# Optimization experiments

Hardware: AMD Instinct MI355X
Metric: run time of the kernel (lower is better)

Reference implementation:

```python
import jax, jax.numpy as jnp
import numpy as np

B, S, HID = 1, 2048, 4096
NH, KVH, D = 32, 8, 128
MAXP = 2048
EPS = 1e-6


def _rope_tables(max_pos, dim, base=10000.0):
    inv_freq = 1.0 / (base ** (np.arange(0, dim, 2, dtype=np.float32) / dim))
    t = np.arange(max_pos, dtype=np.float32)
    freqs = np.outer(t, inv_freq)                      # [max_pos, dim/2]
    emb = np.concatenate([freqs, freqs], axis=-1)      # [max_pos, dim]
    return jnp.asarray(np.cos(emb)), jnp.asarray(np.sin(emb))


def setup_inputs() -> dict:
    key = jax.random.key(0)
    ks = jax.random.split(key, 6)
    x = jax.random.normal(ks[0], (B, S, HID), jnp.float32)
    scale = 0.02
    wq = jax.random.normal(ks[1], (NH * D, HID), jnp.float32) * scale
    wk = jax.random.normal(ks[2], (KVH * D, HID), jnp.float32) * scale
    wv = jax.random.normal(ks[3], (KVH * D, HID), jnp.float32) * scale
    wo = jax.random.normal(ks[4], (NH * D, HID), jnp.float32).T * scale  # stored as [HID, NH*D] -> transpose back
    wo = jnp.asarray(jax.random.normal(ks[4], (HID, NH * D), jnp.float32) * scale)
    cos_table, sin_table = _rope_tables(MAXP, D)
    return {
        "x": x, "wq": wq, "wk": wk, "wv": wv, "wo": wo,
        "q_norm_w": jnp.ones((D,), jnp.float32),
        "k_norm_w": jnp.ones((D,), jnp.float32),
        "cos_table": cos_table, "sin_table": sin_table,
        "k_cache": jnp.zeros((1, B, MAXP, KVH, D), jnp.float32),
        "v_cache": jnp.zeros((1, B, MAXP, KVH, D), jnp.float32),
        "positions": jnp.arange(S, dtype=jnp.int32),
        "layer_idx": 0,
    }


def _rmsnorm(x, w):
    return w * (x * jax.lax.rsqrt(jnp.mean(x * x, axis=-1, keepdims=True) + EPS))


def _rope(x, cos, sin):
    # x: [B, H, S, D]; cos/sin: [1, 1, S, D]
    half = x.shape[-1] // 2
    x1, x2 = x[..., :half], x[..., half:]
    rotated = jnp.concatenate([-x2, x1], axis=-1)
    return x * cos + rotated * sin


def reference(x, wq, wk, wv, wo, q_norm_w, k_norm_w, cos_table, sin_table,
              k_cache, v_cache, positions, layer_idx):
    bsz, seq_len, _ = x.shape
    d = q_norm_w.shape[0]
    nh = wq.shape[0] // d
    kvh = wk.shape[0] // d
    g = nh // kvh

    q = (x @ wq.T).reshape(bsz, seq_len, nh, d).transpose(0, 2, 1, 3)    # [B,NH,S,D]
    k = (x @ wk.T).reshape(bsz, seq_len, kvh, d).transpose(0, 2, 1, 3)   # [B,KVH,S,D]
    v = (x @ wv.T).reshape(bsz, seq_len, kvh, d).transpose(0, 2, 1, 3)

    q = _rmsnorm(q, q_norm_w)
    k = _rmsnorm(k, k_norm_w)

    cos = cos_table[positions][None, None]  # [1,1,S,D]
    sin = sin_table[positions][None, None]
    q = _rope(q, cos, sin)
    k = _rope(k, cos, sin)

    # KV-cache scatter at dynamic positions (prefill: positions = arange(S))
    kc = k_cache[layer_idx].at[:, positions].set(k.transpose(0, 2, 1, 3))
    vc = v_cache[layer_idx].at[:, positions].set(v.transpose(0, 2, 1, 3))
    # K = max(positions)+1 == seq_len in this (prefill) setup; static for jit
    K = seq_len
    k_all = kc[:, :K].transpose(0, 2, 1, 3)   # [B,KVH,K,D]
    v_all = vc[:, :K].transpose(0, 2, 1, 3)

    # GQA: group query heads instead of repeat_interleave on K/V (same math)
    qg = q.reshape(bsz, kvh, g, seq_len, d)
    scale = 1.0 / jnp.sqrt(jnp.asarray(d, q.dtype))
    scores = jnp.einsum('bkgqd,bkld->bkgql', qg, k_all) * scale
    causal = jnp.tril(jnp.ones((seq_len, K), dtype=bool))
    scores = jnp.where(causal, scores, jnp.finfo(scores.dtype).min)
    attn = jax.nn.softmax(scores, axis=-1)
    out = jnp.einsum('bkgql,bkld->bkgqd', attn, v_all)
    out = out.reshape(bsz, nh, seq_len, d).transpose(0, 2, 1, 3).reshape(bsz, seq_len, nh * d)
    return out @ wo.T
```

## Files before the change

### kernel.cpp

```cpp
#include <hip/hip_runtime.h>

typedef unsigned short u16;
typedef unsigned int u32;
typedef __attribute__((ext_vector_type(8))) short bf16x8;
typedef __attribute__((ext_vector_type(4))) float f32x4;
struct __align__(8) us4 { u16 x, y, z, w; };

#define S_LEN 2048
#define HID   4096
#define NH    32
#define KVH   8
#define HD    128
#define MFMA16 __builtin_amdgcn_mfma_f32_16x16x32_bf16

__device__ inline u16 f2bf(float f) {
  u32 u = __float_as_uint(f);
  u32 r = (u + 0x7fffu + ((u >> 16) & 1u)) >> 16;
  return (u16)r;
}
__device__ inline float bf2f(u16 h) { return __uint_as_float(((u32)h) << 16); }

__device__ inline void gld_lds16(const void* g, void* l) {
  __builtin_amdgcn_global_load_lds(
      (const __attribute__((address_space(1))) u32*)g,
      (__attribute__((address_space(3))) u32*)l, 16, 0, 0);
}

__global__ __launch_bounds__(256)
void cvt_all(const float* __restrict__ x, const float* __restrict__ wq,
             const float* __restrict__ wk, const float* __restrict__ wv,
             u16* __restrict__ xb, u16* __restrict__ wqb,
             u16* __restrict__ wkb, u16* __restrict__ wvb) {
  int b = blockIdx.x;
  const float* in; u16* out; int base;
  if (b < 8192)       { in = x;  out = xb;  base = b; }
  else if (b < 24576) { in = wq; out = wqb; base = b - 8192; }
  else if (b < 28672) { in = wk; out = wkb; base = b - 24576; }
  else                { in = wv; out = wvb; base = b - 28672; }
  size_t i = ((size_t)base * 256 + threadIdx.x) * 4;
  f32x4 v = *(const f32x4*)(in + i);
  us4 o;
  o.x = f2bf(v[0]); o.y = f2bf(v[1]); o.z = f2bf(v[2]); o.w = f2bf(v[3]);
  *(us4*)(out + i) = o;
}

__device__ __forceinline__ void stage_half(const u16* __restrict__ src, int ldk,
                                           int rowBase, int k0, char* lslot,
                                           int t) {
  int rl = t >> 3;
  int c8 = ((t & 7) ^ (rl & 7)) * 8;
  gld_lds16(src + (size_t)(rowBase + rl) * ldk + k0 + c8, lslot + t * 16);
  gld_lds16(src + (size_t)(rowBase + 64 + rl) * ldk + k0 + c8,
            lslot + 8192 + t * 16);
}

__device__ __forceinline__ void gemm256_core(
    const u16* __restrict__ A, const u16* __restrict__ W, int m0, int n0,
    int ldk, int kBeg, int kEnd, char* lds, f32x4 (&acc)[8][4]) {
  const int t = threadIdx.x;
  const int l = t & 63, w = t >> 6;
  const int l15 = l & 15, quad = l >> 4;
  const int wr = w >> 2, wcn = w & 3;
  const int nt = (kEnd - kBeg) >> 6;
  char* ldsA = lds;
  char* ldsB = lds + 65536;
  const int swz0 = ((0 + quad) ^ (l15 & 7)) * 16;
  const int swz1 = ((4 + quad) ^ (l15 & 7)) * 16;
  const int aB0 = wr * 16384 + l15 * 128;
  const int bB0 = wcn * 8192 + l15 * 128;

#pragma unroll
  for (int m = 0; m < 8; m++)
#pragma unroll
    for (int n = 0; n < 4; n++) acc[m][n] = (f32x4){0.f, 0.f, 0.f, 0.f};

  stage_half(W, ldk, n0,       kBeg, ldsB,         t);
  stage_half(W, ldk, n0 + 128, kBeg, ldsB + 16384, t);
  stage_half(A, ldk, m0,       kBeg, ldsA,         t);
  stage_half(A, ldk, m0 + 128, kBeg, ldsA + 16384, t);
  if (nt > 1) {
    stage_half(W, ldk, n0,       kBeg + 64, ldsB + 32768,         t);
    stage_half(W, ldk, n0 + 128, kBeg + 64, ldsB + 32768 + 16384, t);
    stage_half(A, ldk, m0,       kBeg + 64, ldsA + 32768,         t);
    stage_half(A, ldk, m0 + 128, kBeg + 64, ldsA + 32768 + 16384, t);
    asm volatile("s_waitcnt vmcnt(8)" ::: "memory");
  } else {
    asm volatile("s_waitcnt vmcnt(0)" ::: "memory");
  }
  __builtin_amdgcn_s_barrier();

  bf16x8 a[4][2], b[2][2], b2[2][2];
#pragma unroll 1
  for (int tt = 0; tt < nt; ++tt) {
    const int d = tt & 1;
    const int aO = d * 32768 + aB0;
    const int bO = d * 32768 + bB0;
    const int k2 = kBeg + (tt + 2) * 64;
    const bool pf = (tt + 2 < nt);

#pragma unroll
    for (int m = 0; m < 4; m++) {
      a[m][0] = *(const bf16x8*)(ldsA + aO + m * 2048 + swz0);
      a[m][1] = *(const bf16x8*)(ldsA + aO + m * 2048 + swz1);
    }
#pragma unroll
    for (int n = 0; n < 2; n++) {
      b[n][0] = *(const bf16x8*)(ldsB + bO + n * 2048 + swz0);
      b[n][1] = *(const bf16x8*)(ldsB + bO + n * 2048 + swz1);
    }
    __builtin_amdgcn_s_barrier();
    __builtin_amdgcn_s_setprio(1);
#pragma unroll
    for (int m = 0; m < 4; m++)
#pragma unroll
      for (int n = 0; n < 2; n++) {
        acc[m][n] = MFMA16(a[m][0], b[n][0], acc[m][n], 0, 0, 0);
        acc[m][n] = MFMA16(a[m][1], b[n][1], acc[m][n], 0, 0, 0);
      }
    __builtin_amdgcn_s_setprio(0);
    __builtin_amdgcn_s_barrier();

#pragma unroll
    for (int n = 0; n < 2; n++) {
      b2[n][0] = *(const bf16x8*)(ldsB + bO + (2 + n) * 2048 + swz0);
      b2[n][1] = *(const bf16x8*)(ldsB + bO + (2 + n) * 2048 + swz1);
    }
    __builtin_amdgcn_s_barrier();
    __builtin_amdgcn_s_setprio(1);
#pragma unroll
    for (int m = 0; m < 4; m++)
#pragma unroll
      for (int n = 0; n < 2; n++) {
        acc[m][2 + n] = MFMA16(a[m][0], b2[n][0], acc[m][2 + n], 0, 0, 0);
        acc[m][2 + n] = MFMA16(a[m][1], b2[n][1], acc[m][2 + n], 0, 0, 0);
      }
    __builtin_amdgcn_s_setprio(0);
    __builtin_amdgcn_s_barrier();

    if (pf) {
      stage_half(W, ldk, n0,       k2, ldsB + d * 32768,         t);
      stage_half(W, ldk, n0 + 128, k2, ldsB + d * 32768 + 16384, t);
    }
#pragma unroll
    for (int m = 0; m < 4; m++) {
      a[m][0] = *(const bf16x8*)(ldsA + aO + (4 + m) * 2048 + swz0);
      a[m][1] = *(const bf16x8*)(ldsA + aO + (4 + m) * 2048 + swz1);
    }
    __builtin_amdgcn_s_barrier();
    __builtin_amdgcn_s_setprio(1);
#pragma unroll
    for (int m = 0; m < 4; m++)
#pragma unroll
      for (int n = 0; n < 2; n++) {
        acc[4 + m][n] = MFMA16(a[m][0], b[n][0], acc[4 + m][n], 0, 0, 0);
        acc[4 + m][n] = MFMA16(a[m][1], b[n][1], acc[4 + m][n], 0, 0, 0);
      }
    __builtin_amdgcn_s_setprio(0);
    __builtin_amdgcn_s_barrier();

    if (pf) {
      stage_half(A, ldk, m0,       k2, ldsA + d * 32768,         t);
      stage_half(A, ldk, m0 + 128, k2, ldsA + d * 32768 + 16384, t);
    }
    __builtin_amdgcn_s_barrier();
    __builtin_amdgcn_s_setprio(1);
#pragma unroll
    for (int m = 0; m < 4; m++)
#pragma unroll
      for (int n = 0; n < 2; n++) {
        acc[4 + m][2 + n] = MFMA16(a[m][0], b2[n][0], acc[4 + m][2 + n], 0, 0, 0);
        acc[4 + m][2 + n] = MFMA16(a[m][1], b2[n][1], acc[4 + m][2 + n], 0, 0, 0);
      }
    __builtin_amdgcn_s_setprio(0);
    if (pf) asm volatile("s_waitcnt vmcnt(8)" ::: "memory");
    else    asm volatile("s_waitcnt vmcnt(0)" ::: "memory");
    __builtin_amdgcn_s_barrier();
  }
}

__global__ __launch_bounds__(512, 2)
void gemm_qkv8(const u16* __restrict__ xb, const u16* __restrict__ wqb,
               const u16* __restrict__ wkb, const u16* __restrict__ wvb,
               u16* __restrict__ Qp, u16* __restrict__ Kp, u16* __restrict__ vt,
               const float* __restrict__ wo, u16* __restrict__ wob) {
  extern __shared__ char lds[];
  const int id = blockIdx.x;
  if (id >= 192) {
    int cb = id - 192;
    size_t base = ((size_t)cb * 512 + threadIdx.x) * 4;
#pragma unroll 1
    for (int it = 0; it < 128; ++it) {
      size_t i = base + (size_t)it * 131072;
      f32x4 v = *(const f32x4*)(wo + i);
      us4 o;
      o.x = f2bf(v[0]); o.y = f2bf(v[1]); o.z = f2bf(v[2]); o.w = f2bf(v[3]);
      *(us4*)(wob + i) = o;
    }
    return;
  }
  const int sw = (id & 7) * 24 + (id >> 3);
  const int bx = sw % 24, by = sw / 24;
  const u16* W; u16* C; int n0, ldc, epi;
  if (bx < 16)      { W = wqb; C = Qp; n0 = bx * 256;        ldc = HID;  epi = 0; }
  else if (bx < 20) { W = wkb; C = Kp; n0 = (bx - 16) * 256; ldc = 1024; epi = 0; }
  else              { W = wvb; C = vt; n0 = (bx - 20) * 256; ldc = 0;    epi = 1; }
  const int m0 = by * 256;

  f32x4 acc[8][4];
  gemm256_core(xb, W, m0, n0, HID, 0, HID, lds, acc);

  const int t = threadIdx.x, l = t & 63, w = t >> 6;
  const int l15 = l & 15, quad = l >> 4;
  const int wr = w >> 2, wcn = w & 3;
  if (epi == 0) {
#pragma unroll
    for (int m = 0; m < 8; m++) {
      int row0 = m0 + wr * 128 + m * 16 + quad * 4;
#pragma unroll
      for (int n = 0; n < 4; n++) {
        int col = n0 + wcn * 64 + n * 16 + l15;
#pragma unroll
        for (int r = 0; r < 4; r++)
          C[(size_t)(row0 + r) * ldc + col] = f2bf(acc[m][n][r]);
      }
    }
  } else {
#pragma unroll
    for (int m = 0; m < 8; m++) {
      int row0 = m0 + wr * 128 + m * 16 + quad * 4;
#pragma unroll
      for (int n = 0; n < 4; n++) {
        int col = n0 + wcn * 64 + n * 16 + l15;
        us4 v;
        v.x = f2bf(acc[m][n][0]); v.y = f2bf(acc[m][n][1]);
        v.z = f2bf(acc[m][n][2]); v.w = f2bf(acc[m][n][3]);
        *(us4*)(vt + (size_t)col * S_LEN + row0) = v;
      }
    }
  }
}

__global__ __launch_bounds__(512, 2)
void gemm_out8(const u16* __restrict__ ab, const u16* __restrict__ wob,
               float* __restrict__ O0, float* __restrict__ O1) {
  extern __shared__ char lds[];
  const int id = blockIdx.x;
  const int sw = (id & 7) * 32 + (id >> 3);
  const int z = sw >> 7, rem = sw & 127;
  const int by = rem >> 4, bx = rem & 15;
  float* Op = z ? O1 : O0;

  f32x4 acc[8][4];
  gemm256_core(ab, wob, by * 256, bx * 256, HID, z * 2048, z * 2048 + 2048, lds, acc);

  const int t = threadIdx.x, l = t & 63, w = t >> 6;
  const int l15 = l & 15, quad = l >> 4;
  const int wr = w >> 2, wcn = w & 3;
#pragma unroll
  for (int m = 0; m < 8; m++) {
    int row0 = by * 256 + wr * 128 + m * 16 + quad * 4;
#pragma unroll
    for (int n = 0; n < 4; n++) {
      int col = bx * 256 + wcn * 64 + n * 16 + l15;
#pragma unroll
      for (int r = 0; r < 4; r++)
        Op[(size_t)(row0 + r) * HID + col] = acc[m][n][r];
    }
  }
}

__global__ __launch_bounds__(256)
void reduce_out(const float* __restrict__ O0, const float* __restrict__ O1,
                float* __restrict__ outp) {
  size_t i = ((size_t)blockIdx.x * 256 + threadIdx.x) * 4;
  f32x4 a = *(const f32x4*)(O0 + i);
  f32x4 b = *(const f32x4*)(O1 + i);
  a[0] += b[0]; a[1] += b[1]; a[2] += b[2]; a[3] += b[3];
  *(f32x4*)(outp + i) = a;
}

__global__ __launch_bounds__(256)
void rope_all(const u16* __restrict__ Qp, const u16* __restrict__ Kp,
              const float* __restrict__ qnw, const float* __restrict__ knw,
              const float* __restrict__ cosT, const float* __restrict__ sinT,
              const int* __restrict__ pos, u16* __restrict__ qbh,
              u16* __restrict__ kbh) {
  const int b = blockIdx.x;
  const int t = threadIdx.x, w = t >> 6, l = t & 63;
  const u16* xr; const float* nw; u16* orow; int s;
  if (b < 16384) {
    int p = b * 4 + w;
    s = p >> 5; int h = p & 31;
    xr = Qp + (size_t)s * HID + h * HD;
    nw = qnw;
    orow = qbh + ((size_t)h * S_LEN + s) * HD;
  } else {
    int p = (b - 16384) * 4 + w;
    s = p >> 3; int h = p & 7;
    xr = Kp + (size_t)s * 1024 + h * HD;
    nw = knw;
    orow = kbh + ((size_t)h * S_LEN + s) * HD;
  }
  float x1 = bf2f(xr[l]);
  float x2 = bf2f(xr[l + 64]);
  float ss = x1 * x1 + x2 * x2;
#pragma unroll
  for (int m = 1; m < 64; m <<= 1) ss += __shfl_xor(ss, m);
  float rinv = rsqrtf(ss * (1.0f / 128.0f) + 1e-6f);
  float n1 = x1 * rinv * nw[l];
  float n2 = x2 * rinv * nw[l + 64];
  int ps = pos[s];
  float c1 = cosT[ps * HD + l], s1 = sinT[ps * HD + l];
  float c2 = cosT[ps * HD + l + 64], s2 = sinT[ps * HD + l + 64];
  float y1 = n1 * c1 - n2 * s1;
  float y2 = n2 * c2 + n1 * s2;
  orow[l] = f2bf(y1);
  orow[l + 64] = f2bf(y2);
}

__global__ __launch_bounds__(256)
void attn_fwd(const u16* __restrict__ qh, const u16* __restrict__ kbh,
              const u16* __restrict__ vth, u16* __restrict__ ab) {
  __shared__ __align__(16) u16 lK[64 * 128];
  __shared__ __align__(16) u16 lV[128 * 64];
  __shared__ __align__(16) u16 lP[4][16 * 72];
  const int t = threadIdx.x, w = t >> 6, l = t & 63;
  const int quad = l >> 4, l15 = l & 15;
  const int h = blockIdx.x;
  const int qt = 31 - blockIdx.y;
  const int kvh = h >> 2;
  const int q0 = qt * 64;
  const int qrow = q0 + w * 16 + l15;

  bf16x8 qf[4];
#pragma unroll
  for (int ks = 0; ks < 4; ks++)
    qf[ks] = *(const bf16x8*)(qh + ((size_t)h * S_LEN + qrow) * HD + ks * 32 + quad * 8);

  f32x4 accO[8];
#pragma unroll
  for (int j = 0; j < 8; j++) accO[j] = (f32x4){0.f, 0.f, 0.f, 0.f};
  float m_cur = -3.0e38f, l_sum = 0.f;
  const float scale = 0.08838834764831845f;

  const int ntiles = qt + 1;
  for (int tt = 0; tt < ntiles; tt++) {
    const int c0 = tt * 64;
#pragma unroll
    for (int i = 0; i < 4; i++) {
      int Cc = i * 256 + t;
      int r = Cc >> 4, ch = Cc & 15;
      int gch = ch ^ (r & 15);
      gld_lds16(kbh + ((size_t)kvh * S_LEN + c0 + r) * HD + gch * 8, lK + Cc * 8);
    }
#pragma unroll
    for (int i = 0; i < 4; i++) {
      int Cc = i * 256 + t;
      int d = Cc >> 3, ch = Cc & 7;
      int gch = ch ^ (d & 7);
      gld_lds16(vth + ((size_t)kvh * HD + d) * S_LEN + c0 + gch * 8, lV + Cc * 8);
    }
    __syncthreads();

    f32x4 st[4];
#pragma unroll
    for (int i = 0; i < 4; i++) {
      f32x4 sa = (f32x4){0.f, 0.f, 0.f, 0.f};
      int r = i * 16 + l15;
#pragma unroll
      for (int ks = 0; ks < 4; ks++) {
        int lc = ks * 4 + quad;
        bf16x8 kf = *(const bf16x8*)(lK + r * 128 + ((lc ^ (r & 15)) * 8));
        sa = __builtin_amdgcn_mfma_f32_16x16x32_bf16(kf, qf[ks], sa, 0, 0, 0);
      }
      st[i] = sa;
    }

    float tmax = -3.0e38f;
#pragma unroll
    for (int i = 0; i < 4; i++) {
#pragma unroll
      for (int r = 0; r < 4; r++) {
        int kcol = c0 + i * 16 + quad * 4 + r;
        float v = st[i][r] * scale;
        v = (kcol <= qrow) ? v : -3.0e38f;
        st[i][r] = v;
        tmax = fmaxf(tmax, v);
      }
    }
    tmax = fmaxf(tmax, __shfl_xor(tmax, 16));
    tmax = fmaxf(tmax, __shfl_xor(tmax, 32));
    float m_new = fmaxf(m_cur, tmax);
    float alpha = __expf(m_cur - m_new);

    float psum = 0.f;
#pragma unroll
    for (int i = 0; i < 4; i++) {
      us4 pv;
      u16* pp = (u16*)&pv;
#pragma unroll
      for (int r = 0; r < 4; r++) {
        float pe = __expf(st[i][r] - m_new);
        psum += pe;
        pp[r] = f2bf(pe);
      }
      *(us4*)(&lP[w][l15 * 72 + i * 16 + quad * 4]) = pv;
    }
    psum += __shfl_xor(psum, 16);
    psum += __shfl_xor(psum, 32);
    l_sum = l_sum * alpha + psum;
    m_cur = m_new;

#pragma unroll
    for (int r = 0; r < 4; r++) {
      float ar = __shfl(alpha, quad * 4 + r);
#pragma unroll
      for (int j = 0; j < 8; j++) accO[j][r] *= ar;
    }

    bf16x8 pf[2];
#pragma unroll
    for (int ks = 0; ks < 2; ks++)
      pf[ks] = *(const bf16x8*)(&lP[w][l15 * 72 + ks * 32 + quad * 8]);
#pragma unroll
    for (int j = 0; j < 8; j++) {
      int d = j * 16 + l15;
#pragma unroll
      for (int ks = 0; ks < 2; ks++) {
        int lc = ks * 4 + quad;
        bf16x8 vf = *(const bf16x8*)(lV + d * 64 + ((lc ^ (d & 7)) * 8));
        accO[j] = __builtin_amdgcn_mfma_f32_16x16x32_bf16(pf[ks], vf, accO[j], 0, 0, 0);
      }
    }
    __syncthreads();
  }

  float linv = 1.0f / l_sum;
#pragma unroll
  for (int r = 0; r < 4; r++) {
    float lr = __shfl(linv, quad * 4 + r);
    int row = q0 + w * 16 + quad * 4 + r;
#pragma unroll
    for (int j = 0; j < 8; j++) {
      int col = h * HD + j * 16 + l15;
      ab[(size_t)row * HID + col] = f2bf(accO[j][r] * lr);
    }
  }
}

extern "C" void kernel_launch(void* const* d_in, const int* in_sizes, int n_in,
                              void* d_out, int out_size, void* d_ws, size_t ws_size,
                              hipStream_t stream) {
  const float* x    = (const float*)d_in[0];
  const float* wq   = (const float*)d_in[1];
  const float* wk   = (const float*)d_in[2];
  const float* wv   = (const float*)d_in[3];
  const float* wo   = (const float*)d_in[4];
  const float* qnw  = (const float*)d_in[5];
  const float* knw  = (const float*)d_in[6];
  const float* cosT = (const float*)d_in[7];
  const float* sinT = (const float*)d_in[8];
  const int* positions = (const int*)d_in[11];

  static int attr_done = 0;
  if (!attr_done) {
    hipFuncSetAttribute((const void*)gemm_qkv8,
                        hipFuncAttributeMaxDynamicSharedMemorySize, 131072);
    hipFuncSetAttribute((const void*)gemm_out8,
                        hipFuncAttributeMaxDynamicSharedMemorySize, 131072);
    attr_done = 1;
  }

  char* ws = (char*)d_ws;
  u16* xb  = (u16*)(ws + 0ULL);
  u16* wqb = (u16*)(ws + 16777216ULL);
  u16* wkb = (u16*)(ws + 50331648ULL);
  u16* wvb = (u16*)(ws + 58720256ULL);
  u16* wob = (u16*)(ws + 67108864ULL);
  u16* Qp  = (u16*)(ws + 100663296ULL);
  u16* Kp  = (u16*)(ws + 117440512ULL);
  u16* vt  = (u16*)(ws + 121634816ULL);
  u16* qbh = (u16*)(ws + 125829120ULL);
  u16* kbh = (u16*)(ws + 142606336ULL);
  u16* ab  = (u16*)(ws + 146800640ULL);
  float* O0 = (float*)(ws + 0ULL);
  float* O1 = (float*)(ws + 33554432ULL);

  cvt_all<<<32768, 256, 0, stream>>>(x, wq, wk, wv, xb, wqb, wkb, wvb);

  gemm_qkv8<<<256, 512, 131072, stream>>>(xb, wqb, wkb, wvb, Qp, Kp, vt, wo, wob);

  rope_all<<<20480, 256, 0, stream>>>(Qp, Kp, qnw, knw, cosT, sinT, positions,
                                      qbh, kbh);

  attn_fwd<<<dim3(NH, S_LEN / 64), 256, 0, stream>>>(qbh, kbh, vt, ab);

  gemm_out8<<<256, 512, 131072, stream>>>(ab, wob, O0, O1);
  reduce_out<<<8192, 256, 0, stream>>>(O0, O1, (float*)d_out);
}
```

Baseline: 492.7 us.

## Retile fused QKV GEMM to 256x192 tiles and move wo conversion into attention

Places the bf16 Wq/Wk/Wv contiguously so the QKV projection becomes one GEMM over 6144 output columns. That GEMM gets a dedicated kernel with 256x192 tiles, giving exactly 256 equal blocks instead of 192 GEMM blocks plus 64 conversion blocks. The fp32-to-bf16 conversion of wo moves from the QKV GEMM launch into extra blocks of the attention kernel, where it overlaps with the causally imbalanced attention tiles. This trades a new, hand-pipelined GEMM loop with a different LDS budget for better load balance, at the risk of lower per-block efficiency.

```diff
diff --git a/kernel.cpp b/kernel.cpp
--- a/kernel.cpp
+++ b/kernel.cpp
@@ -29,19 +29,26 @@
 __global__ __launch_bounds__(256)
 void cvt_all(const float* __restrict__ x, const float* __restrict__ wq,
              const float* __restrict__ wk, const float* __restrict__ wv,
-             u16* __restrict__ xb, u16* __restrict__ wqb,
-             u16* __restrict__ wkb, u16* __restrict__ wvb) {
+             u16* __restrict__ xb, u16* __restrict__ wqkvb) {
   int b = blockIdx.x;
   const float* in; u16* out; int base;
-  if (b < 8192)       { in = x;  out = xb;  base = b; }
-  else if (b < 24576) { in = wq; out = wqb; base = b - 8192; }
-  else if (b < 28672) { in = wk; out = wkb; base = b - 24576; }
-  else                { in = wv; out = wvb; base = b - 28672; }
+  if (b < 8192)       { in = x;  out = xb;                    base = b; }
+  else if (b < 24576) { in = wq; out = wqkvb;                 base = b - 8192; }
+  else if (b < 28672) { in = wk; out = wqkvb + 16777216;      base = b - 24576; }
+  else                { in = wv; out = wqkvb + 20971520;      base = b - 28672; }
   size_t i = ((size_t)base * 256 + threadIdx.x) * 4;
   f32x4 v = *(const f32x4*)(in + i);
   us4 o;
   o.x = f2bf(v[0]); o.y = f2bf(v[1]); o.z = f2bf(v[2]); o.w = f2bf(v[3]);
   *(us4*)(out + i) = o;
+}
+
+__device__ __forceinline__ void stage_slab(const u16* __restrict__ src, int ldk,
+                                           int rowBase, int k0, char* lslot,
+                                           int t) {
+  int rl = t >> 3;
+  int c8 = ((t & 7) ^ (rl & 7)) * 8;
+  gld_lds16(src + (size_t)(rowBase + rl) * ldk + k0 + c8, lslot + t * 16);
 }
 
 __device__ __forceinline__ void stage_half(const u16* __restrict__ src, int ldk,
@@ -52,6 +59,155 @@
   gld_lds16(src + (size_t)(rowBase + rl) * ldk + k0 + c8, lslot + t * 16);
   gld_lds16(src + (size_t)(rowBase + 64 + rl) * ldk + k0 + c8,
             lslot + 8192 + t * 16);
+}
+
+__global__ __launch_bounds__(512, 2)
+void gemm_qkv8(const u16* __restrict__ xb, const u16* __restrict__ wqkvb,
+               u16* __restrict__ Qp, u16* __restrict__ Kp, u16* __restrict__ vt) {
+  extern __shared__ char lds[];
+  const int id = blockIdx.x;
+  const int sw = (id & 7) * 32 + (id >> 3);
+  const int by = sw >> 5, bx = sw & 31;
+  const int m0 = by * 256, n0 = bx * 192;
+  const int t = threadIdx.x;
+  const int l = t & 63, w = t >> 6;
+  const int l15 = l & 15, quad = l >> 4;
+  const int wr = w >> 1, wcn = w & 1;
+  char* ldsA = lds;
+  char* ldsB = lds + 65536;
+  const int swz0 = ((0 + quad) ^ (l15 & 7)) * 16;
+  const int swz1 = ((4 + quad) ^ (l15 & 7)) * 16;
+  const int aB0 = wr * 8192 + l15 * 128;
+  const int bB0 = wcn * 12288 + l15 * 128;
+  const int nt = HID / 64;
+
+  f32x4 acc[4][6];
+#pragma unroll
+  for (int m = 0; m < 4; m++)
+#pragma unroll
+    for (int n = 0; n < 6; n++) acc[m][n] = (f32x4){0.f, 0.f, 0.f, 0.f};
+
+#pragma unroll
+  for (int s = 0; s < 3; s++) stage_slab(wqkvb, HID, n0 + s * 64, 0, ldsB + s * 8192, t);
+#pragma unroll
+  for (int s = 0; s < 4; s++) stage_slab(xb, HID, m0 + s * 64, 0, ldsA + s * 8192, t);
+#pragma unroll
+  for (int s = 0; s < 3; s++) stage_slab(wqkvb, HID, n0 + s * 64, 64, ldsB + 24576 + s * 8192, t);
+  asm volatile("s_waitcnt vmcnt(3)" ::: "memory");
+  __builtin_amdgcn_s_barrier();
+
+  bf16x8 a[2][2], a2[2][2], b[3][2], b2[3][2];
+#pragma unroll 1
+  for (int tt = 0; tt < nt; ++tt) {
+    const int d = tt & 1, dn = d ^ 1;
+    const int aO = d * 32768 + aB0;
+    const int bO = d * 24576 + bB0;
+    const int k1 = (tt + 1) * 64, k2 = (tt + 2) * 64;
+    const bool pf1 = (tt + 1 < nt), pf2 = (tt + 2 < nt);
+
+#pragma unroll
+    for (int m = 0; m < 2; m++) {
+      a[m][0] = *(const bf16x8*)(ldsA + aO + m * 2048 + swz0);
+      a[m][1] = *(const bf16x8*)(ldsA + aO + m * 2048 + swz1);
+    }
+#pragma unroll
+    for (int n = 0; n < 3; n++) {
+      b[n][0] = *(const bf16x8*)(ldsB + bO + n * 2048 + swz0);
+      b[n][1] = *(const bf16x8*)(ldsB + bO + n * 2048 + swz1);
+    }
+    if (pf1) {
+      stage_slab(xb, HID, m0,      k1, ldsA + dn * 32768,        t);
+      stage_slab(xb, HID, m0 + 64, k1, ldsA + dn * 32768 + 8192, t);
+    }
+    __builtin_amdgcn_s_barrier();
+    __builtin_amdgcn_s_setprio(1);
+#pragma unroll
+    for (int m = 0; m < 2; m++)
+#pragma unroll
+      for (int n = 0; n < 3; n++) {
+        acc[m][n] = MFMA16(a[m][0], b[n][0], acc[m][n], 0, 0, 0);
+        acc[m][n] = MFMA16(a[m][1], b[n][1], acc[m][n], 0, 0, 0);
+      }
+    __builtin_amdgcn_s_setprio(0);
+    __builtin_amdgcn_s_barrier();
+
+#pragma unroll
+    for (int n = 0; n < 3; n++) {
+      b2[n][0] = *(const bf16x8*)(ldsB + bO + (3 + n) * 2048 + swz0);
+      b2[n][1] = *(const bf16x8*)(ldsB + bO + (3 + n) * 2048 + swz1);
+    }
+    if (pf1) {
+      stage_slab(xb, HID, m0 + 128, k1, ldsA + dn * 32768 + 16384, t);
+      stage_slab(xb, HID, m0 + 192, k1, ldsA + dn * 32768 + 24576, t);
+    }
+    __builtin_amdgcn_s_barrier();
+    __builtin_amdgcn_s_setprio(1);
+#pragma unroll
+    for (int m = 0; m < 2; m++)
+#pragma unroll
+      for (int n = 0; n < 3; n++) {
+        acc[m][3 + n] = MFMA16(a[m][0], b2[n][0], acc[m][3 + n], 0, 0, 0);
+        acc[m][3 + n] = MFMA16(a[m][1], b2[n][1], acc[m][3 + n], 0, 0, 0);
+      }
+    __builtin_amdgcn_s_setprio(0);
+    __builtin_amdgcn_s_barrier();
+
+#pragma unroll
+    for (int m = 0; m < 2; m++) {
+      a2[m][0] = *(const bf16x8*)(ldsA + aO + (2 + m) * 2048 + swz0);
+      a2[m][1] = *(const bf16x8*)(ldsA + aO + (2 + m) * 2048 + swz1);
+    }
+    if (pf2) {
+#pragma unroll
+      for (int s = 0; s < 3; s++)
+        stage_slab(wqkvb, HID, n0 + s * 64, k2, ldsB + d * 24576 + s * 8192, t);
+    }
+    __builtin_amdgcn_s_barrier();
+    __builtin_amdgcn_s_setprio(1);
+#pragma unroll
+    for (int m = 0; m < 2; m++)
+#pragma unroll
+      for (int n = 0; n < 3; n++) {
+        acc[2 + m][n] = MFMA16(a2[m][0], b[n][0], acc[2 + m][n], 0, 0, 0);
+        acc[2 + m][n] = MFMA16(a2[m][1], b[n][1], acc[2 + m][n], 0, 0, 0);
+      }
+#pragma unroll
+    for (int m = 0; m < 2; m++)
+#pragma unroll
+      for (int n = 0; n < 3; n++) {
+        acc[2 + m][3 + n] = MFMA16(a2[m][0], b2[n][0], acc[2 + m][3 + n], 0, 0, 0);
+        acc[2 + m][3 + n] = MFMA16(a2[m][1], b2[n][1], acc[2 + m][3 + n], 0, 0, 0);
+      }
+    __builtin_amdgcn_s_setprio(0);
+    if (pf1) {
+      if (pf2) asm volatile("s_waitcnt vmcnt(3)" ::: "memory");
+      else     asm volatile("s_waitcnt vmcnt(0)" ::: "memory");
+      __builtin_amdgcn_s_barrier();
+    }
+  }
+
+#pragma unroll
+  for (int m = 0; m < 4; m++) {
+    int row0 = m0 + wr * 64 + m * 16 + quad * 4;
+#pragma unroll
+    for (int n = 0; n < 6; n++) {
+      int col = n0 + wcn * 96 + n * 16 + l15;
+      if (col < 4096) {
+#pragma unroll
+        for (int r = 0; r < 4; r++)
+          Qp[(size_t)(row0 + r) * HID + col] = f2bf(acc[m][n][r]);
+      } else if (col < 5120) {
+#pragma unroll
+        for (int r = 0; r < 4; r++)
+          Kp[(size_t)(row0 + r) * 1024 + (col - 4096)] = f2bf(acc[m][n][r]);
+      } else {
+        us4 v;
+        v.x = f2bf(acc[m][n][0]); v.y = f2bf(acc[m][n][1]);
+        v.z = f2bf(acc[m][n][2]); v.w = f2bf(acc[m][n][3]);
+        *(us4*)(vt + (size_t)(col - 5120) * S_LEN + row0) = v;
+      }
+    }
+  }
 }
 
 __device__ __forceinline__ void gemm256_core(
@@ -175,68 +331,6 @@
     if (pf) asm volatile("s_waitcnt vmcnt(8)" ::: "memory");
     else    asm volatile("s_waitcnt vmcnt(0)" ::: "memory");
     __builtin_amdgcn_s_barrier();
-  }
-}
-
-__global__ __launch_bounds__(512, 2)
-void gemm_qkv8(const u16* __restrict__ xb, const u16* __restrict__ wqb,
-               const u16* __restrict__ wkb, const u16* __restrict__ wvb,
-               u16* __restrict__ Qp, u16* __restrict__ Kp, u16* __restrict__ vt,
-               const float* __restrict__ wo, u16* __restrict__ wob) {
-  extern __shared__ char lds[];
-  const int id = blockIdx.x;
-  if (id >= 192) {
-    int cb = id - 192;
-    size_t base = ((size_t)cb * 512 + threadIdx.x) * 4;
-#pragma unroll 1
-    for (int it = 0; it < 128; ++it) {
-      size_t i = base + (size_t)it * 131072;
-      f32x4 v = *(const f32x4*)(wo + i);
-      us4 o;
-      o.x = f2bf(v[0]); o.y = f2bf(v[1]); o.z = f2bf(v[2]); o.w = f2bf(v[3]);
-      *(us4*)(wob + i) = o;
-    }
-    return;
-  }
-  const int sw = (id & 7) * 24 + (id >> 3);
-  const int bx = sw % 24, by = sw / 24;
-  const u16* W; u16* C; int n0, ldc, epi;
-  if (bx < 16)      { W = wqb; C = Qp; n0 = bx * 256;        ldc = HID;  epi = 0; }
-  else if (bx < 20) { W = wkb; C = Kp; n0 = (bx - 16) * 256; ldc = 1024; epi = 0; }
-  else              { W = wvb; C = vt; n0 = (bx - 20) * 256; ldc = 0;    epi = 1; }
-  const int m0 = by * 256;
-
-  f32x4 acc[8][4];
-  gemm256_core(xb, W, m0, n0, HID, 0, HID, lds, acc);
-
-  const int t = threadIdx.x, l = t & 63, w = t >> 6;
-  const int l15 = l & 15, quad = l >> 4;
-  const int wr = w >> 2, wcn = w & 3;
-  if (epi == 0) {
-#pragma unroll
-    for (int m = 0; m < 8; m++) {
-      int row0 = m0 + wr * 128 + m * 16 + quad * 4;
-#pragma unroll
-      for (int n = 0; n < 4; n++) {
-        int col = n0 + wcn * 64 + n * 16 + l15;
-#pragma unroll
-        for (int r = 0; r < 4; r++)
-          C[(size_t)(row0 + r) * ldc + col] = f2bf(acc[m][n][r]);
-      }
-    }
-  } else {
-#pragma unroll
-    for (int m = 0; m < 8; m++) {
-      int row0 = m0 + wr * 128 + m * 16 + quad * 4;
-#pragma unroll
-      for (int n = 0; n < 4; n++) {
-        int col = n0 + wcn * 64 + n * 16 + l15;
-        us4 v;
-        v.x = f2bf(acc[m][n][0]); v.y = f2bf(acc[m][n][1]);
-        v.z = f2bf(acc[m][n][2]); v.w = f2bf(acc[m][n][3]);
-        *(us4*)(vt + (size_t)col * S_LEN + row0) = v;
-      }
-    }
   }
 }
 
@@ -320,12 +414,24 @@
 
 __global__ __launch_bounds__(256)
 void attn_fwd(const u16* __restrict__ qh, const u16* __restrict__ kbh,
-              const u16* __restrict__ vth, u16* __restrict__ ab) {
+              const u16* __restrict__ vth, u16* __restrict__ ab,
+              const float* __restrict__ wo, u16* __restrict__ wob) {
   __shared__ __align__(16) u16 lK[64 * 128];
   __shared__ __align__(16) u16 lV[128 * 64];
   __shared__ __align__(16) u16 lP[4][16 * 72];
   const int t = threadIdx.x, w = t >> 6, l = t & 63;
   const int quad = l >> 4, l15 = l & 15;
+  if (blockIdx.x >= NH) {
+    int cb = (blockIdx.x - NH) * 32 + blockIdx.y;
+    for (size_t i = (size_t)cb * 256 + t; i < 4194304; i += 98304) {
+      size_t j = i * 4;
+      f32x4 v = *(const f32x4*)(wo + j);
+      us4 o;
+      o.x = f2bf(v[0]); o.y = f2bf(v[1]); o.z = f2bf(v[2]); o.w = f2bf(v[3]);
+      *(us4*)(wob + j) = o;
+    }
+    return;
+  }
   const int h = blockIdx.x;
   const int qt = 31 - blockIdx.y;
   const int kvh = h >> 2;
@@ -465,35 +571,34 @@
   static int attr_done = 0;
   if (!attr_done) {
     hipFuncSetAttribute((const void*)gemm_qkv8,
-                        hipFuncAttributeMaxDynamicSharedMemorySize, 131072);
+                        hipFuncAttributeMaxDynamicSharedMemorySize, 114688);
     hipFuncSetAttribute((const void*)gemm_out8,
                         hipFuncAttributeMaxDynamicSharedMemorySize, 131072);
     attr_done = 1;
   }
 
   char* ws = (char*)d_ws;
-  u16* xb  = (u16*)(ws + 0ULL);
-  u16* wqb = (u16*)(ws + 16777216ULL);
-  u16* wkb = (u16*)(ws + 50331648ULL);
-  u16* wvb = (u16*)(ws + 58720256ULL);
-  u16* wob = (u16*)(ws + 67108864ULL);
-  u16* Qp  = (u16*)(ws + 100663296ULL);
-  u16* Kp  = (u16*)(ws + 117440512ULL);
-  u16* vt  = (u16*)(ws + 121634816ULL);
-  u16* qbh = (u16*)(ws + 125829120ULL);
-  u16* kbh = (u16*)(ws + 142606336ULL);
-  u16* ab  = (u16*)(ws + 146800640ULL);
-  float* O0 = (float*)(ws + 0ULL);
-  float* O1 = (float*)(ws + 33554432ULL);
-
-  cvt_all<<<32768, 256, 0, stream>>>(x, wq, wk, wv, xb, wqb, wkb, wvb);
-
-  gemm_qkv8<<<256, 512, 131072, stream>>>(xb, wqb, wkb, wvb, Qp, Kp, vt, wo, wob);
+  u16* xb    = (u16*)(ws + 0ULL);
+  u16* wqkvb = (u16*)(ws + 16777216ULL);
+  u16* wob   = (u16*)(ws + 67108864ULL);
+  u16* Qp    = (u16*)(ws + 100663296ULL);
+  u16* Kp    = (u16*)(ws + 117440512ULL);
+  u16* vt    = (u16*)(ws + 121634816ULL);
+  u16* qbh   = (u16*)(ws + 125829120ULL);
+  u16* kbh   = (u16*)(ws + 142606336ULL);
+  u16* ab    = (u16*)(ws + 146800640ULL);
+  float* O0  = (float*)(ws + 0ULL);
+  float* O1  = (float*)(ws + 33554432ULL);
+
+  cvt_all<<<32768, 256, 0, stream>>>(x, wq, wk, wv, xb, wqkvb);
+
+  gemm_qkv8<<<256, 512, 114688, stream>>>(xb, wqkvb, Qp, Kp, vt);
 
   rope_all<<<20480, 256, 0, stream>>>(Qp, Kp, qnw, knw, cosT, sinT, positions,
                                       qbh, kbh);
 
-  attn_fwd<<<dim3(NH, S_LEN / 64), 256, 0, stream>>>(qbh, kbh, vt, ab);
+  attn_fwd<<<dim3(NH + 12, S_LEN / 64), 256, 0, stream>>>(qbh, kbh, vt, ab,
+                                                          wo, wob);
 
   gemm_out8<<<256, 512, 131072, stream>>>(ab, wob, O0, O1);
   reduce_out<<<8192, 256, 0, stream>>>(O0, O1, (float*)d_out);
```

Result: no change. 491.8 us (-0.2%).
